# Kernel optimization log

Measured on AMD Instinct MI355X. Metric: run time of the kernel, lower is better.

## Reference

```python
import jax, jax.numpy as jnp
import numpy as np
from jax import lax

DN = ('NCHW', 'OIHW', 'NCHW')

def _conv(x, w, b):
    y = lax.conv_general_dilated(x, w, (1, 1), 'SAME', dimension_numbers=DN)
    return y + b[None, :, None, None]

def setup_inputs() -> dict:
    key = jax.random.key(0)
    ks = jax.random.split(key, 12)
    B, C, H, W = 8, 32, 128, 128
    Cb, INT, K, FK = 64, 64, 3, 3
    inp = {
        'z': jax.random.normal(ks[0], (B, C, H, W), jnp.float32),
        'backbone': jax.random.normal(ks[1], (B, Cb, H, W), jnp.float32),
        'mem_stab': jax.random.normal(ks[2], (B, C, H, W), jnp.float32),
        'mem_unstab': jax.random.normal(ks[3], (B, C, H, W), jnp.float32),
        'w0': jax.random.normal(ks[4], (INT, Cb + 3 * C, K, K), jnp.float32) * 0.05,
        'b0': jnp.zeros((INT,), jnp.float32),
        'w1': jax.random.normal(ks[5], (INT, INT, K, K), jnp.float32) * 0.05,
        'b1': jnp.zeros((INT,), jnp.float32),
        'w2': jax.random.normal(ks[6], (INT, INT, K, K), jnp.float32) * 0.05,
        'b2': jnp.zeros((INT,), jnp.float32),
        'w_last': jax.random.normal(ks[7], (C * FK * FK, INT, K, K), jnp.float32) * 0.05,
        'b_last': jnp.full((C * FK * FK,), -4.0, jnp.float32),
        'fusion_kernel_size': FK,
    }
    return inp

def reference(z, backbone, mem_stab, mem_unstab, w0, b0, w1, b1, w2, b2, w_last, b_last, fusion_kernel_size):
    B, C, H, W = z.shape
    k = int(fusion_kernel_size)
    p = k * k
    # controller conv stack (LeakyReLU slope 0.01, matching nn.LeakyReLU default)
    q = jnp.concatenate([backbone, z, mem_stab, mem_unstab], axis=1)
    q = jax.nn.leaky_relu(_conv(q, w0, b0), 0.01)
    q = jax.nn.leaky_relu(_conv(q, w1, b1), 0.01)
    q = jax.nn.leaky_relu(_conv(q, w2, b2), 0.01)
    # fusion head -> [B, C, p, HW]
    head = _conv(q, w_last, b_last).reshape(B, C, p, H * W)
    # softmax over p kernel positions + one extra logit-0 slot for z itself
    eta = jax.nn.softmax(jnp.concatenate([head, jnp.zeros_like(head[:, :, :1])], axis=2), axis=2)
    # unfold(mem_stab, k, padding=k//2): patches ordered (c, kh, kw) like torch unfold
    pad = k // 2
    mpad = jnp.pad(mem_stab, ((0, 0), (0, 0), (pad, pad), (pad, pad)))
    patches = jnp.stack([mpad[:, :, i:i + H, j:j + W] for i in range(k) for j in range(k)], axis=2)
    patches = patches.reshape(B, C, p, H * W)
    z_flat = z.reshape(B, C, H * W)
    z_stab = (patches * eta[:, :, :p]).sum(axis=2) + eta[:, :, p] * z_flat
    return z_stab.reshape(B, C, H, W)
```

## Files before the change

kernel.cpp:

```cpp
#include <hip/hip_runtime.h>
#include <hip/hip_fp16.h>

typedef _Float16 half8 __attribute__((ext_vector_type(8)));
typedef _Float16 half4v __attribute__((ext_vector_type(4)));
typedef float floatx4 __attribute__((ext_vector_type(4)));

#define HW 128
#define IMG (HW * HW)
#define PH 130
#define WP 200
#define XP 164

typedef __attribute__((address_space(3))) _Float16 lds_f16;
typedef __attribute__((address_space(1))) const _Float16 glb_f16;
__device__ __forceinline__ void gload16(const _Float16* g, _Float16* l) {
    __builtin_amdgcn_global_load_lds((glb_f16*)g, (lds_f16*)l, 16, 0, 0);
}

__global__ void pack_w_all(const float* __restrict__ w0, const float* __restrict__ w1,
                           const float* __restrict__ w2, const float* __restrict__ wl,
                           _Float16* __restrict__ p0, _Float16* __restrict__ p1,
                           _Float16* __restrict__ p2, _Float16* __restrict__ pl) {
    int idx = blockIdx.x * 256 + threadIdx.x;
    if (idx < 92160) {
        int local = idx;
        int o = local / 1440;
        int rem = local % 1440;
        int c = rem / 9;
        int t = rem % 9;
        int oh = o >> 5, n = (o >> 4) & 1, l15 = o & 15;
        int cb = c >> 5, l4 = (c >> 3) & 3, e = c & 7;
        int frag = (t * 5 + cb) * 2 + n;
        p0[(size_t)oh * 46080 + frag * 512 + (l4 * 16 + l15) * 8 + e] =
            (_Float16)w0[local];
        return;
    }
    if (idx < 165888) {
        const float* w; _Float16* p; int local;
        if (idx < 129024) { w = w1; p = p1; local = idx - 92160; }
        else              { w = w2; p = p2; local = idx - 129024; }
        int o = local / 576;
        int rem = local % 576;
        int c = rem / 9;
        int t = rem % 9;
        int r = t / 3, dw = t % 3;
        p[((size_t)r * 64 + o) * 192 + (dw * 8 + (c >> 3)) * 8 + (c & 7)] =
            (_Float16)w[local];
        return;
    }
    if (idx < 331776) {
        int local = idx - 165888;
        int og = local / 576;
        int rem = local % 576;
        int c = rem / 9;
        int t = rem % 9;
        int ct = og / 96, o = og % 96;
        int r = t / 3, dw = t % 3;
        int kk = dw * 8 + (c >> 3);
        int ks = (kk & 0x18) | ((kk & 7) ^ (o & 7));
        pl[(((size_t)ct * 3 + r) * 96 + o) * 192 + ks * 8 + (c & 7)] =
            (_Float16)wl[local];
    }
}

__device__ __forceinline__ void zero_halo(_Float16* P, int C, int id) {
    int nvec = C / 8;
    int b = id / (516 * nvec);
    int r = id % (516 * nvec);
    int cell = r / nvec;
    int v = r % nvec;
    int hh, ww;
    if (cell < 130)      { hh = 0;   ww = cell; }
    else if (cell < 260) { hh = 129; ww = cell - 130; }
    else if (cell < 388) { hh = cell - 260 + 1; ww = 0; }
    else                 { hh = cell - 388 + 1; ww = 129; }
    half8 z8 = {};
    *reinterpret_cast<half8*>(P + (((size_t)b * PH + hh) * PH + ww) * C + v * 8) = z8;
}

__global__ void zero_pads_pre(_Float16* __restrict__ X0, _Float16* __restrict__ Q1) {
    int id = blockIdx.x * 256 + threadIdx.x;
    if (id < 82560) zero_halo(X0, 160, id);
    else if (id < 115584) zero_halo(Q1, 64, id - 82560);
}

__global__ void zero_pads64(_Float16* __restrict__ P) {
    int id = blockIdx.x * 256 + threadIdx.x;
    if (id < 33024) zero_halo(P, 64, id);
}

__global__ __launch_bounds__(256)
void pack_in(const float* __restrict__ z, const float* __restrict__ bb,
             const float* __restrict__ ms, const float* __restrict__ mu,
             _Float16* __restrict__ X0) {
    __shared__ _Float16 lds[160 * 132];
    int b = blockIdx.x >> 7;
    int h = blockIdx.x & 127;
    int tid = threadIdx.x;

    for (int i = 0; i < 20; i++) {
        int id = i * 256 + tid;
        int c = id >> 5;
        int col = (id & 31) * 4;
        const float* src; int cs; int csz;
        if (c < 64)       { src = bb; cs = c;       csz = 64; }
        else if (c < 96)  { src = z;  cs = c - 64;  csz = 32; }
        else if (c < 128) { src = ms; cs = c - 96;  csz = 32; }
        else              { src = mu; cs = c - 128; csz = 32; }
        float4 v = *reinterpret_cast<const float4*>(
            src + ((size_t)b * csz + cs) * IMG + h * HW + col);
        half4v hv = { (_Float16)v.x, (_Float16)v.y, (_Float16)v.z, (_Float16)v.w };
        *reinterpret_cast<half4v*>(&lds[c * 132 + col]) = hv;
    }
    __syncthreads();
    _Float16* dst = X0 + (((size_t)b * PH + (h + 1)) * PH + 1) * 160;
    for (int i = 0; i < 10; i++) {
        int id = i * 256 + tid;
        int pix = id / 20;
        int c0 = (id % 20) * 8;
        half8 hv;
        #pragma unroll
        for (int e = 0; e < 8; e++) hv[e] = lds[(c0 + e) * 132 + pix];
        *reinterpret_cast<half8*>(dst + (size_t)pix * 160 + c0) = hv;
    }
}

__global__ __launch_bounds__(256, 2)
void conv3_c160(const _Float16* __restrict__ X, const _Float16* __restrict__ Wp,
                const float* __restrict__ bias, _Float16* __restrict__ Y) {
    __shared__ _Float16 xs[130 * XP];
    int b = blockIdx.x >> 7;
    int h = blockIdx.x & 127;
    int tid = threadIdx.x;
    int lane = tid & 63;
    int wave = tid >> 6;
    int ph = wave & 1;
    int oh = wave >> 1;
    int l15 = lane & 15;
    int l4  = lane >> 4;

    floatx4 acc[4][2] = {};
    half8 SA[10], SB[10];

    const _Float16* wl = Wp + (size_t)oh * 46080 + lane * 8;

#define LOADW(S, k) { \
    _Pragma("unroll") \
    for (int cb = 0; cb < 5; cb++) \
      _Pragma("unroll") \
      for (int n = 0; n < 2; n++) \
        S[cb * 2 + n] = *reinterpret_cast<const half8*>( \
            wl + (size_t)(((k) * 5 + cb) * 2 + n) * 512); }

#define STAGE160(r) { \
    const _Float16* grow = X + ((size_t)b * PH + (h + (r))) * PH * 160; \
    _Pragma("unroll") \
    for (int i = 0; i < 11; i++) { \
      int id = i * 256 + tid; \
      if (id < 2600) { \
        half8 v = *reinterpret_cast<const half8*>(grow + (size_t)id * 8); \
        *reinterpret_cast<half8*>(&xs[(id / 20) * XP + (id % 20) * 8]) = v; \
      } } }

#define COMP160(dw, S) { \
    _Pragma("unroll") \
    for (int cb = 0; cb < 5; cb++) { \
      int kofs = cb * 32 + l4 * 8; \
      half8 af[4]; \
      _Pragma("unroll") \
      for (int m = 0; m < 4; m++) { \
        int p = ph * 64 + m * 16 + l15; \
        af[m] = *reinterpret_cast<const half8*>(&xs[(p + (dw)) * XP + kofs]); \
      } \
      _Pragma("unroll") \
      for (int m = 0; m < 4; m++) \
        _Pragma("unroll") \
        for (int n = 0; n < 2; n++) \
          acc[m][n] = __builtin_amdgcn_mfma_f32_16x16x32_f16( \
              af[m], S[cb * 2 + n], acc[m][n], 0, 0, 0); } }

    LOADW(SA, 0);
    STAGE160(0);
    __syncthreads();
    LOADW(SB, 1);  COMP160(0, SA);
    LOADW(SA, 2);  COMP160(1, SB);
    LOADW(SB, 3);  COMP160(2, SA);
    __syncthreads();
    STAGE160(1);
    __syncthreads();
    LOADW(SA, 4);  COMP160(0, SB);
    LOADW(SB, 5);  COMP160(1, SA);
    LOADW(SA, 6);  COMP160(2, SB);
    __syncthreads();
    STAGE160(2);
    __syncthreads();
    LOADW(SB, 7);  COMP160(0, SA);
    LOADW(SA, 8);  COMP160(1, SB);
    COMP160(2, SA);

#undef LOADW
#undef STAGE160
#undef COMP160

    _Float16* dst = Y + (((size_t)b * PH + (h + 1)) * PH + 1) * 64;
    #pragma unroll
    for (int m = 0; m < 4; m++)
        #pragma unroll
        for (int n = 0; n < 2; n++) {
            int o = oh * 32 + n * 16 + l15;
            float bv = bias[o];
            #pragma unroll
            for (int q = 0; q < 4; q++) {
                int pix = ph * 64 + m * 16 + l4 * 4 + q;
                float v = acc[m][n][q] + bv;
                v = v > 0.f ? v : 0.01f * v;
                dst[(size_t)pix * 64 + o] = (_Float16)v;
            }
        }
}

__global__ __launch_bounds__(256, 3)
void conv3_c64(const _Float16* __restrict__ X, const _Float16* __restrict__ Wp,
               const float* __restrict__ bias, _Float16* __restrict__ Y) {
    __shared__ _Float16 smem[9360 + 64 * WP];
    _Float16* xs = smem;
    _Float16* wbuf = smem + 9360;
    int b = blockIdx.x >> 7;
    int h = blockIdx.x & 127;
    int tid = threadIdx.x;
    int lane = tid & 63;
    int wave = tid >> 6;
    int ph = wave & 1;
    int oh = wave >> 1;
    int l15 = lane & 15;
    int l4  = lane >> 4;

    floatx4 acc[4][2] = {};
    const _Float16* xbase = X + ((size_t)b * PH + h) * (PH * 64);

    for (int r = 0; r < 3; r++) {
        if (r) __syncthreads();
        for (int i = 0; i < 5; i++) {
            int id = i * 256 + tid;
            if (id < 1040) {
                half8 v = *reinterpret_cast<const half8*>(
                    xbase + (size_t)r * (PH * 64) + (size_t)id * 8);
                *reinterpret_cast<half8*>(&xs[(id >> 3) * 72 + (id & 7) * 8]) = v;
            }
        }
        const _Float16* wr = Wp + (size_t)r * 12288;
        for (int i = 0; i < 6; i++) {
            int id = i * 256 + tid;
            int o = id / 24, j = id % 24;
            half8 v = *reinterpret_cast<const half8*>(wr + (size_t)id * 8);
            *reinterpret_cast<half8*>(&wbuf[o * WP + j * 8]) = v;
        }
        __syncthreads();
        #pragma unroll
        for (int dw = 0; dw < 3; dw++)
            #pragma unroll
            for (int cb = 0; cb < 2; cb++) {
                int kofs = cb * 32 + l4 * 8;
                half8 bf[2];
                #pragma unroll
                for (int n = 0; n < 2; n++) {
                    int o = oh * 32 + n * 16 + l15;
                    bf[n] = *reinterpret_cast<const half8*>(
                        &wbuf[o * WP + dw * 64 + kofs]);
                }
                half8 af[4];
                #pragma unroll
                for (int m = 0; m < 4; m++) {
                    int p = ph * 64 + m * 16 + l15;
                    af[m] = *reinterpret_cast<const half8*>(&xs[(p + dw) * 72 + kofs]);
                }
                #pragma unroll
                for (int m = 0; m < 4; m++)
                    #pragma unroll
                    for (int n = 0; n < 2; n++)
                        acc[m][n] = __builtin_amdgcn_mfma_f32_16x16x32_f16(
                            af[m], bf[n], acc[m][n], 0, 0, 0);
            }
    }
    _Float16* dst = Y + (((size_t)b * PH + (h + 1)) * PH + 1) * 64;
    #pragma unroll
    for (int m = 0; m < 4; m++)
        #pragma unroll
        for (int n = 0; n < 2; n++) {
            int o = oh * 32 + n * 16 + l15;
            float bv = bias[o];
            #pragma unroll
            for (int q = 0; q < 4; q++) {
                int pix = ph * 64 + m * 16 + l4 * 4 + q;
                float v = acc[m][n][q] + bv;
                v = v > 0.f ? v : 0.01f * v;
                dst[(size_t)pix * 64 + o] = (_Float16)v;
            }
        }
}

__global__ __launch_bounds__(256, 3)
void head_gemm(const _Float16* __restrict__ X, const _Float16* __restrict__ Wp,
               const float* __restrict__ b_last, _Float16* __restrict__ Lg,
               int bbase) {
    __shared__ _Float16 smem[26752];
    _Float16* xs = smem;
    _Float16* wbuf = smem + 8320;
    _Float16* tb = smem;
    int blk = blockIdx.x;
    int ct = blk >> 9;
    int bi = (blk >> 7) & 3;
    int h  = blk & 127;
    int b = bbase + bi;
    int tid = threadIdx.x;
    int lane = tid & 63;
    int wave = tid >> 6;
    int pxh = wave & 1;
    int og  = wave >> 1;
    int l15 = lane & 15;
    int l4  = lane >> 4;

    floatx4 acc[4][3] = {};
    const _Float16* xbase = X + ((size_t)b * PH + h) * (PH * 64);
    const _Float16* wbase = Wp + (size_t)ct * 55296;

    for (int r = 0; r < 3; r++) {
        if (r) __syncthreads();
        const _Float16* xrow = xbase + (size_t)r * (PH * 64);
        for (int i = 0; i < 5; i++) {
            int sbase = i * 256 + wave * 64;
            int s = sbase + lane;
            if (s < 1040) {
                int px = s >> 3;
                int j = (s & 7) ^ (px & 7);
                gload16(xrow + (size_t)(px * 8 + j) * 8, xs + (size_t)sbase * 8);
            }
        }
        const _Float16* wrow = wbase + (size_t)r * 18432;
        for (int i = 0; i < 9; i++) {
            int tbs = i * 256 + wave * 64;
            int t = tbs + lane;
            gload16(wrow + (size_t)t * 8, wbuf + (size_t)tbs * 8);
        }
        __syncthreads();
        #pragma unroll
        for (int dw = 0; dw < 3; dw++)
            #pragma unroll
            for (int cb = 0; cb < 2; cb++) {
                int kb = dw * 8 + cb * 4 + l4;
                half8 bf[3];
                #pragma unroll
                for (int n = 0; n < 3; n++) {
                    int ol = og * 48 + n * 16 + l15;
                    int ksw = (kb & 0x18) | ((kb & 7) ^ (ol & 7));
                    bf[n] = *reinterpret_cast<const half8*>(&wbuf[ol * 192 + ksw * 8]);
                }
                int j = cb * 4 + l4;
                half8 af[4];
                #pragma unroll
                for (int m = 0; m < 4; m++) {
                    int px = pxh * 64 + m * 16 + l15 + dw;
                    af[m] = *reinterpret_cast<const half8*>(
                        &xs[px * 64 + (j ^ (px & 7)) * 8]);
                }
                #pragma unroll
                for (int m = 0; m < 4; m++)
                    #pragma unroll
                    for (int n = 0; n < 3; n++)
                        acc[m][n] = __builtin_amdgcn_mfma_f32_16x16x32_f16(
                            af[m], bf[n], acc[m][n], 0, 0, 0);
            }
    }
    __syncthreads();

    #pragma unroll
    for (int m = 0; m < 4; m++)
        #pragma unroll
        for (int n = 0; n < 3; n++) {
            int od = og * 48 + n * 16 + l15;
            float bv = b_last[ct * 96 + od];
            half4v hv;
            #pragma unroll
            for (int q = 0; q < 4; q++) hv[q] = (_Float16)(acc[m][n][q] + bv);
            *reinterpret_cast<half4v*>(&tb[od * 132 + pxh * 64 + m * 16 + l4 * 4]) = hv;
        }
    __syncthreads();

    _Float16* dst = Lg + (((size_t)bi * 128 + h) * 288 + (size_t)ct * 96) * 128;
    #pragma unroll
    for (int i = 0; i < 6; i++) {
        int id = i * 256 + tid;
        int od = id >> 4;
        int sl = id & 15;
        half8 v = *reinterpret_cast<const half8*>(&tb[od * 132 + sl * 8]);
        *reinterpret_cast<half8*>(dst + (size_t)od * 128 + sl * 8) = v;
    }
}

__global__ __launch_bounds__(256)
void fuse_sm(const _Float16* __restrict__ Lg, const float* __restrict__ ms,
             const float* __restrict__ zin, float* __restrict__ out, int bbase) {
    int blk = blockIdx.x;
    int bi = blk >> 11;
    int c  = (blk >> 6) & 31;
    int hp = blk & 63;
    int tid = threadIdx.x;
    int h = hp * 2 + (tid >> 7);
    int w = tid & 127;
    int b = bbase + bi;

    const _Float16* lrow = Lg + (((size_t)bi * 128 + h) * 288 + (size_t)c * 9) * 128 + w;
    float L[9];
    float mx = 0.f;
    #pragma unroll
    for (int j = 0; j < 9; j++) { L[j] = (float)lrow[j * 128]; mx = fmaxf(mx, L[j]); }
    float ez = __expf(-mx);
    float sum = ez;
    float e[9];
    #pragma unroll
    for (int j = 0; j < 9; j++) { e[j] = __expf(L[j] - mx); sum += e[j]; }
    float inv = 1.f / sum;
    const float* msb = ms + ((size_t)b * 32 + c) * IMG;
    float accv = ez * inv * zin[((size_t)b * 32 + c) * IMG + h * HW + w];
    #pragma unroll
    for (int kh = 0; kh < 3; kh++) {
        int h2 = h + kh - 1;
        int h2c = min(max(h2, 0), 127);
        bool okh = (unsigned)h2 < 128u;
        #pragma unroll
        for (int kw = 0; kw < 3; kw++) {
            int w2 = w + kw - 1;
            int w2c = min(max(w2, 0), 127);
            bool okw = (unsigned)w2 < 128u;
            float mv = msb[h2c * HW + w2c];
            accv += e[kh * 3 + kw] * inv * ((okh && okw) ? mv : 0.f);
        }
    }
    out[((size_t)b * 32 + c) * IMG + h * HW + w] = accv;
}

extern "C" void kernel_launch(void* const* d_in, const int* in_sizes, int n_in,
                              void* d_out, int out_size, void* d_ws, size_t ws_size,
                              hipStream_t stream) {
    const float* z  = (const float*)d_in[0];
    const float* bb = (const float*)d_in[1];
    const float* ms = (const float*)d_in[2];
    const float* mu = (const float*)d_in[3];
    const float* w0 = (const float*)d_in[4];
    const float* b0 = (const float*)d_in[5];
    const float* w1 = (const float*)d_in[6];
    const float* b1 = (const float*)d_in[7];
    const float* w2 = (const float*)d_in[8];
    const float* b2 = (const float*)d_in[9];
    const float* wl = (const float*)d_in[10];
    const float* bl = (const float*)d_in[11];

    char* ws = (char*)d_ws;
    _Float16* Wp0 = (_Float16*)(ws + 0);
    _Float16* Wp1 = (_Float16*)(ws + 184320);
    _Float16* Wp2 = (_Float16*)(ws + 258048);
    _Float16* WpL = (_Float16*)(ws + 331776);
    _Float16* BufA = (_Float16*)(ws + 663552);
    _Float16* BufB = (_Float16*)(ws + 43927552);

    _Float16* X0 = BufA;
    _Float16* Q1 = BufB;
    _Float16* Q2 = BufA;
    _Float16* Q3 = BufB;
    _Float16* Lg = BufA;

    pack_w_all<<<(331776 + 255) / 256, 256, 0, stream>>>(w0, w1, w2, wl, Wp0, Wp1, Wp2, WpL);
    zero_pads_pre<<<(115584 + 255) / 256, 256, 0, stream>>>(X0, Q1);
    pack_in<<<1024, 256, 0, stream>>>(z, bb, ms, mu, X0);

    conv3_c160<<<1024, 256, 0, stream>>>(X0, Wp0, b0, Q1);
    zero_pads64<<<(33024 + 255) / 256, 256, 0, stream>>>(Q2);
    conv3_c64<<<1024, 256, 0, stream>>>(Q1, Wp1, b1, Q2);
    conv3_c64<<<1024, 256, 0, stream>>>(Q2, Wp2, b2, Q3);

    head_gemm<<<1536, 256, 0, stream>>>(Q3, WpL, bl, Lg, 0);
    fuse_sm<<<8192, 256, 0, stream>>>(Lg, ms, z, (float*)d_out, 0);
    head_gemm<<<1536, 256, 0, stream>>>(Q3, WpL, bl, Lg, 4);
    fuse_sm<<<8192, 256, 0, stream>>>(Lg, ms, z, (float*)d_out, 4);
}
```

Measured before the change: 188.7 us.

## Load conv weights directly into registers in fragment layout, drop LDS weight staging

Weights for conv3_c64 and head_gemm are repacked into per-lane MFMA fragment order so each wave reads its B fragments straight from global memory into registers, double-buffered one step ahead of the MFMAs. This removes the LDS weight buffers and their staging loads, cuts shared memory per block, and unrolls the three-row loop explicitly. Launch bounds drop from 3 to 2 blocks per CU to leave room for the extra registers, which may reduce occupancy and expose global-load latency on weight fetches.

```diff
diff --git a/kernel.cpp b/kernel.cpp
--- a/kernel.cpp
+++ b/kernel.cpp
@@ -8,7 +8,6 @@
 #define HW 128
 #define IMG (HW * HW)
 #define PH 130
-#define WP 200
 #define XP 164
 
 typedef __attribute__((address_space(3))) _Float16 lds_f16;
@@ -43,23 +42,28 @@
         int rem = local % 576;
         int c = rem / 9;
         int t = rem % 9;
-        int r = t / 3, dw = t % 3;
-        p[((size_t)r * 64 + o) * 192 + (dw * 8 + (c >> 3)) * 8 + (c & 7)] =
+        int oh = o >> 5, n = (o >> 4) & 1, l15 = o & 15;
+        int cb = c >> 5, l4 = (c >> 3) & 3, e = c & 7;
+        int frag = t * 4 + cb * 2 + n;
+        p[(size_t)oh * 18432 + frag * 512 + (l4 * 16 + l15) * 8 + e] =
             (_Float16)w[local];
         return;
     }
     if (idx < 331776) {
         int local = idx - 165888;
-        int og = local / 576;
+        int of = local / 576;
         int rem = local % 576;
         int c = rem / 9;
         int t = rem % 9;
-        int ct = og / 96, o = og % 96;
-        int r = t / 3, dw = t % 3;
-        int kk = dw * 8 + (c >> 3);
-        int ks = (kk & 0x18) | ((kk & 7) ^ (o & 7));
-        pl[(((size_t)ct * 3 + r) * 96 + o) * 192 + ks * 8 + (c & 7)] =
-            (_Float16)wl[local];
+        int ct = of / 96, o = of % 96;
+        int og = o / 48;
+        int n = (o % 48) / 16;
+        int l15 = o & 15;
+        int j = c >> 3;
+        int cb = j >> 2, l4 = j & 3, e = c & 7;
+        int frag = t * 2 + cb;
+        pl[((((size_t)(ct * 2 + og) * 18 + frag) * 3 + n) * 64
+            + (l4 * 16 + l15)) * 8 + e] = (_Float16)wl[local];
     }
 }
 
@@ -219,12 +223,10 @@
         }
 }
 
-__global__ __launch_bounds__(256, 3)
+__global__ __launch_bounds__(256, 2)
 void conv3_c64(const _Float16* __restrict__ X, const _Float16* __restrict__ Wp,
                const float* __restrict__ bias, _Float16* __restrict__ Y) {
-    __shared__ _Float16 smem[9360 + 64 * WP];
-    _Float16* xs = smem;
-    _Float16* wbuf = smem + 9360;
+    __shared__ _Float16 xs[130 * 72];
     int b = blockIdx.x >> 7;
     int h = blockIdx.x & 127;
     int tid = threadIdx.x;
@@ -236,52 +238,69 @@
     int l4  = lane >> 4;
 
     floatx4 acc[4][2] = {};
+    half8 SA[4], SB[4];
+
+    const _Float16* wl = Wp + (size_t)oh * 18432 + lane * 8;
     const _Float16* xbase = X + ((size_t)b * PH + h) * (PH * 64);
 
-    for (int r = 0; r < 3; r++) {
-        if (r) __syncthreads();
-        for (int i = 0; i < 5; i++) {
-            int id = i * 256 + tid;
-            if (id < 1040) {
-                half8 v = *reinterpret_cast<const half8*>(
-                    xbase + (size_t)r * (PH * 64) + (size_t)id * 8);
-                *reinterpret_cast<half8*>(&xs[(id >> 3) * 72 + (id & 7) * 8]) = v;
-            }
-        }
-        const _Float16* wr = Wp + (size_t)r * 12288;
-        for (int i = 0; i < 6; i++) {
-            int id = i * 256 + tid;
-            int o = id / 24, j = id % 24;
-            half8 v = *reinterpret_cast<const half8*>(wr + (size_t)id * 8);
-            *reinterpret_cast<half8*>(&wbuf[o * WP + j * 8]) = v;
-        }
-        __syncthreads();
-        #pragma unroll
-        for (int dw = 0; dw < 3; dw++)
-            #pragma unroll
-            for (int cb = 0; cb < 2; cb++) {
-                int kofs = cb * 32 + l4 * 8;
-                half8 bf[2];
-                #pragma unroll
-                for (int n = 0; n < 2; n++) {
-                    int o = oh * 32 + n * 16 + l15;
-                    bf[n] = *reinterpret_cast<const half8*>(
-                        &wbuf[o * WP + dw * 64 + kofs]);
-                }
-                half8 af[4];
-                #pragma unroll
-                for (int m = 0; m < 4; m++) {
-                    int p = ph * 64 + m * 16 + l15;
-                    af[m] = *reinterpret_cast<const half8*>(&xs[(p + dw) * 72 + kofs]);
-                }
-                #pragma unroll
-                for (int m = 0; m < 4; m++)
-                    #pragma unroll
-                    for (int n = 0; n < 2; n++)
-                        acc[m][n] = __builtin_amdgcn_mfma_f32_16x16x32_f16(
-                            af[m], bf[n], acc[m][n], 0, 0, 0);
-            }
-    }
+#define LOADW1(S, k) { \
+    _Pragma("unroll") \
+    for (int cb = 0; cb < 2; cb++) \
+      _Pragma("unroll") \
+      for (int n = 0; n < 2; n++) \
+        S[cb * 2 + n] = *reinterpret_cast<const half8*>( \
+            wl + (size_t)((k) * 4 + cb * 2 + n) * 512); }
+
+#define STAGE64(r) { \
+    const _Float16* grow = xbase + (size_t)(r) * (PH * 64); \
+    _Pragma("unroll") \
+    for (int i = 0; i < 5; i++) { \
+      int id = i * 256 + tid; \
+      if (id < 1040) { \
+        half8 v = *reinterpret_cast<const half8*>(grow + (size_t)id * 8); \
+        *reinterpret_cast<half8*>(&xs[(id >> 3) * 72 + (id & 7) * 8]) = v; \
+      } } }
+
+#define COMP64(dw, S) { \
+    _Pragma("unroll") \
+    for (int cb = 0; cb < 2; cb++) { \
+      int kofs = cb * 32 + l4 * 8; \
+      half8 af[4]; \
+      _Pragma("unroll") \
+      for (int m = 0; m < 4; m++) { \
+        int p = ph * 64 + m * 16 + l15; \
+        af[m] = *reinterpret_cast<const half8*>(&xs[(p + (dw)) * 72 + kofs]); \
+      } \
+      _Pragma("unroll") \
+      for (int m = 0; m < 4; m++) \
+        _Pragma("unroll") \
+        for (int n = 0; n < 2; n++) \
+          acc[m][n] = __builtin_amdgcn_mfma_f32_16x16x32_f16( \
+              af[m], S[cb * 2 + n], acc[m][n], 0, 0, 0); } }
+
+    LOADW1(SA, 0);
+    STAGE64(0);
+    __syncthreads();
+    LOADW1(SB, 1);  COMP64(0, SA);
+    LOADW1(SA, 2);  COMP64(1, SB);
+    LOADW1(SB, 3);  COMP64(2, SA);
+    __syncthreads();
+    STAGE64(1);
+    __syncthreads();
+    LOADW1(SA, 4);  COMP64(0, SB);
+    LOADW1(SB, 5);  COMP64(1, SA);
+    LOADW1(SA, 6);  COMP64(2, SB);
+    __syncthreads();
+    STAGE64(2);
+    __syncthreads();
+    LOADW1(SB, 7);  COMP64(0, SA);
+    LOADW1(SA, 8);  COMP64(1, SB);
+    COMP64(2, SA);
+
+#undef LOADW1
+#undef STAGE64
+#undef COMP64
+
     _Float16* dst = Y + (((size_t)b * PH + (h + 1)) * PH + 1) * 64;
     #pragma unroll
     for (int m = 0; m < 4; m++)
@@ -299,13 +318,12 @@
         }
 }
 
-__global__ __launch_bounds__(256, 3)
+__global__ __launch_bounds__(256, 2)
 void head_gemm(const _Float16* __restrict__ X, const _Float16* __restrict__ Wp,
                const float* __restrict__ b_last, _Float16* __restrict__ Lg,
                int bbase) {
-    __shared__ _Float16 smem[26752];
+    __shared__ _Float16 smem[12672];
     _Float16* xs = smem;
-    _Float16* wbuf = smem + 8320;
     _Float16* tb = smem;
     int blk = blockIdx.x;
     int ct = blk >> 9;
@@ -321,56 +339,77 @@
     int l4  = lane >> 4;
 
     floatx4 acc[4][3] = {};
+    half8 SA[3], SB[3];
+
+    const _Float16* wlh = Wp + ((size_t)ct * 2 + og) * 27648 + lane * 8;
     const _Float16* xbase = X + ((size_t)b * PH + h) * (PH * 64);
-    const _Float16* wbase = Wp + (size_t)ct * 55296;
-
-    for (int r = 0; r < 3; r++) {
-        if (r) __syncthreads();
-        const _Float16* xrow = xbase + (size_t)r * (PH * 64);
-        for (int i = 0; i < 5; i++) {
-            int sbase = i * 256 + wave * 64;
-            int s = sbase + lane;
-            if (s < 1040) {
-                int px = s >> 3;
-                int j = (s & 7) ^ (px & 7);
-                gload16(xrow + (size_t)(px * 8 + j) * 8, xs + (size_t)sbase * 8);
-            }
-        }
-        const _Float16* wrow = wbase + (size_t)r * 18432;
-        for (int i = 0; i < 9; i++) {
-            int tbs = i * 256 + wave * 64;
-            int t = tbs + lane;
-            gload16(wrow + (size_t)t * 8, wbuf + (size_t)tbs * 8);
-        }
-        __syncthreads();
-        #pragma unroll
-        for (int dw = 0; dw < 3; dw++)
-            #pragma unroll
-            for (int cb = 0; cb < 2; cb++) {
-                int kb = dw * 8 + cb * 4 + l4;
-                half8 bf[3];
-                #pragma unroll
-                for (int n = 0; n < 3; n++) {
-                    int ol = og * 48 + n * 16 + l15;
-                    int ksw = (kb & 0x18) | ((kb & 7) ^ (ol & 7));
-                    bf[n] = *reinterpret_cast<const half8*>(&wbuf[ol * 192 + ksw * 8]);
-                }
-                int j = cb * 4 + l4;
-                half8 af[4];
-                #pragma unroll
-                for (int m = 0; m < 4; m++) {
-                    int px = pxh * 64 + m * 16 + l15 + dw;
-                    af[m] = *reinterpret_cast<const half8*>(
-                        &xs[px * 64 + (j ^ (px & 7)) * 8]);
-                }
-                #pragma unroll
-                for (int m = 0; m < 4; m++)
-                    #pragma unroll
-                    for (int n = 0; n < 3; n++)
-                        acc[m][n] = __builtin_amdgcn_mfma_f32_16x16x32_f16(
-                            af[m], bf[n], acc[m][n], 0, 0, 0);
-            }
-    }
+
+#define LOADWH(S, k, cb) { \
+    _Pragma("unroll") \
+    for (int n = 0; n < 3; n++) \
+      S[n] = *reinterpret_cast<const half8*>( \
+          wlh + (size_t)(((k) * 2 + (cb)) * 3 + n) * 512); }
+
+#define STAGEH(r) { \
+    const _Float16* xrow = xbase + (size_t)(r) * (PH * 64); \
+    _Pragma("unroll") \
+    for (int i = 0; i < 5; i++) { \
+      int sbase = i * 256 + wave * 64; \
+      int s = sbase + lane; \
+      if (s < 1040) { \
+        int px = s >> 3; \
+        int j = (s & 7) ^ (px & 7); \
+        gload16(xrow + (size_t)(px * 8 + j) * 8, xs + (size_t)sbase * 8); \
+      } } }
+
+#define COMPH(dw, cb, S) { \
+    int j = (cb) * 4 + l4; \
+    half8 af[4]; \
+    _Pragma("unroll") \
+    for (int m = 0; m < 4; m++) { \
+      int px = pxh * 64 + m * 16 + l15 + (dw); \
+      af[m] = *reinterpret_cast<const half8*>( \
+          &xs[px * 64 + (j ^ (px & 7)) * 8]); \
+    } \
+    _Pragma("unroll") \
+    for (int m = 0; m < 4; m++) \
+      _Pragma("unroll") \
+      for (int n = 0; n < 3; n++) \
+        acc[m][n] = __builtin_amdgcn_mfma_f32_16x16x32_f16( \
+            af[m], S[n], acc[m][n], 0, 0, 0); }
+
+    LOADWH(SA, 0, 0);
+    STAGEH(0);
+    __syncthreads();
+    LOADWH(SB, 0, 1);  COMPH(0, 0, SA);
+    LOADWH(SA, 1, 0);  COMPH(0, 1, SB);
+    LOADWH(SB, 1, 1);  COMPH(1, 0, SA);
+    LOADWH(SA, 2, 0);  COMPH(1, 1, SB);
+    LOADWH(SB, 2, 1);  COMPH(2, 0, SA);
+    LOADWH(SA, 3, 0);  COMPH(2, 1, SB);
+    __syncthreads();
+    STAGEH(1);
+    __syncthreads();
+    LOADWH(SB, 3, 1);  COMPH(0, 0, SA);
+    LOADWH(SA, 4, 0);  COMPH(0, 1, SB);
+    LOADWH(SB, 4, 1);  COMPH(1, 0, SA);
+    LOADWH(SA, 5, 0);  COMPH(1, 1, SB);
+    LOADWH(SB, 5, 1);  COMPH(2, 0, SA);
+    LOADWH(SA, 6, 0);  COMPH(2, 1, SB);
+    __syncthreads();
+    STAGEH(2);
+    __syncthreads();
+    LOADWH(SB, 6, 1);  COMPH(0, 0, SA);
+    LOADWH(SA, 7, 0);  COMPH(0, 1, SB);
+    LOADWH(SB, 7, 1);  COMPH(1, 0, SA);
+    LOADWH(SA, 8, 0);  COMPH(1, 1, SB);
+    LOADWH(SB, 8, 1);  COMPH(2, 0, SA);
+    COMPH(2, 1, SB);
+
+#undef LOADWH
+#undef STAGEH
+#undef COMPH
+
     __syncthreads();
 
     #pragma unroll
```

Measured after the change: 181.7 us. 1.04x faster.
